# Kernel optimization log

Hardware: AMD Instinct MI355X
Metric: run time of the kernel (lower is better)

## Reference

```python
import jax, jax.numpy as jnp
import numpy as np

V_BOOK, V_AUTH, V_LANG, V_TAG = 10001, 5001, 28, 34253
D = 32  # EMBED_DIM
B, C, LH, LW = 4096, 100, 200, 50


def setup_inputs() -> dict:
    key = jax.random.key(0)
    ks = jax.random.split(key, 32)
    it = iter(ks)

    def emb(k, v):
        t = jax.random.normal(k, (v, D), jnp.float32) * 0.05
        return t.at[0].set(0.0)  # padding_idx=0

    def lin(k, i, o):
        k1, k2 = jax.random.split(k)
        lim = 1.0 / np.sqrt(i)
        return (jax.random.uniform(k1, (i, o), jnp.float32, -lim, lim),
                jax.random.uniform(k2, (o,), jnp.float32, -lim, lim))

    hist = jax.random.randint(next(it), (B, LH), 0, V_BOOK)
    wish = jax.random.randint(next(it), (B, LW), 0, V_BOOK)
    cand = jax.random.randint(next(it), (B, C), 0, V_BOOK)
    auth = jax.random.randint(next(it), (B, C), 0, V_AUTH)
    lang = jax.random.randint(next(it), (B, C), 0, V_LANG)
    tags = jax.random.randint(next(it), (B, C, 5), 0, V_TAG)
    dense = jax.random.normal(next(it), (B, C, 3), jnp.float32)

    E_hist = emb(next(it), V_BOOK)
    E_wish = emb(next(it), V_BOOK)
    E_cand = emb(next(it), V_BOOK)
    E_auth = emb(next(it), V_AUTH)
    E_lang = emb(next(it), V_LANG)
    E_tags = emb(next(it), V_TAG)

    Wb0, bb0 = lin(next(it), 3, 32)
    Wb1, bb1 = lin(next(it), 32, D)
    Wt0, bt0 = lin(next(it), 2 * D, 256)
    Wt1, bt1 = lin(next(it), 256, 128)
    Wt2, bt2 = lin(next(it), 128, 64)
    Wt3, bt3 = lin(next(it), 64, 1)

    return dict(hist=hist, wish=wish, cand=cand, auth=auth, lang=lang, tags=tags,
                dense=dense, E_hist=E_hist, E_wish=E_wish, E_cand=E_cand,
                E_auth=E_auth, E_lang=E_lang, E_tags=E_tags,
                Wb0=Wb0, bb0=bb0, Wb1=Wb1, bb1=bb1,
                Wt0=Wt0, bt0=bt0, Wt1=Wt1, bt1=bt1,
                Wt2=Wt2, bt2=bt2, Wt3=Wt3, bt3=bt3)


def reference(hist, wish, cand, auth, lang, tags, dense,
              E_hist, E_wish, E_cand, E_auth, E_lang, E_tags,
              Wb0, bb0, Wb1, bb1, Wt0, bt0, Wt1, bt1, Wt2, bt2, Wt3, bt3):
    # user side: mean-pooled history + wishlist embeddings  [B, D]
    u_vec = E_hist[hist].mean(axis=1) + E_wish[wish].mean(axis=1)
    # item side: candidate + author + language + mean of 5 tag embeddings  [B, C, D]
    e_t = E_tags[tags].sum(axis=2) / 5.0
    i_vec = E_cand[cand] + E_auth[auth] + E_lang[lang] + e_t
    # bottom MLP on dense features  [B, C, D]
    h = jax.nn.relu(jnp.einsum('bcf,fh->bch', dense, Wb0) + bb0)
    d_vec = jnp.einsum('bch,hd->bcd', h, Wb1) + bb1
    i_final = i_vec + d_vec
    # concat broadcast user vec with item vec  [B, C, 2D]
    u_exp = jnp.broadcast_to(u_vec[:, None, :], (u_vec.shape[0], i_final.shape[1], u_vec.shape[1]))
    x = jnp.concatenate([u_exp, i_final], axis=2)
    # top MLP -> scores [B, C]
    x = jax.nn.relu(x @ Wt0 + bt0)
    x = jax.nn.relu(x @ Wt1 + bt1)
    x = jax.nn.relu(x @ Wt2 + bt2)
    scores = (x @ Wt3 + bt3)[..., 0]
    return scores
```

## Files before the change

kernel.cpp:

```cpp
#include <hip/hip_runtime.h>
#include <hip/hip_bf16.h>
#include <stdint.h>

#define NB 4096
#define NC 100
#define NROWS (NB*NC)
#define NTILES (NROWS/64)
#define GRID_F 768
#define LH 200
#define LW 50

typedef short v8s __attribute__((ext_vector_type(8)));
typedef float v4f __attribute__((ext_vector_type(4)));
typedef float v2f __attribute__((ext_vector_type(2)));

__device__ __forceinline__ v4f mfma16(v8s a, v8s b, v4f c) {
  return __builtin_amdgcn_mfma_f32_16x16x32_bf16(a, b, c, 0, 0, 0);
}

__device__ __forceinline__ uint32_t pkbf(float lo, float hi) {
  uint32_t r;
  asm("v_cvt_pk_bf16_f32 %0, %1, %2" : "=v"(r) : "v"(lo), "v"(hi));
  return r;
}

__device__ __forceinline__ uint16_t bf16r(float f) {
  uint32_t u = __builtin_bit_cast(uint32_t, f);
  u = (u + 0x7fffu + ((u >> 16) & 1u)) >> 16;
  return (uint16_t)u;
}

__device__ __forceinline__ float bf2f(short s) {
  return __builtin_bit_cast(float, (uint32_t)((uint16_t)s) << 16);
}

__device__ __forceinline__ int ntli(const int* p) { return __builtin_nontemporal_load(p); }
__device__ __forceinline__ float ntlf(const float* p) { return __builtin_nontemporal_load(p); }

#define WS_FW 524288
#define FRAG_B1 0
#define FRAG_T0 2
#define FRAG_T1 34
#define FRAG_T2 98
#define NFRAGS 114

__global__ void k_prep(const float* __restrict__ Wb1, const float* __restrict__ Wt0,
                       const float* __restrict__ Wt1, const float* __restrict__ Wt2,
                       uint16_t* __restrict__ fb) {
  int f = blockIdx.x;
  int t = threadIdx.x;
  uint16_t res[2];
  #pragma unroll
  for (int e2 = 0; e2 < 2; ++e2) {
    int e = t * 2 + e2;
    int l = e >> 3, i = e & 7;
    int lr = l & 15, lg = l >> 4;
    float v;
    if (f < FRAG_T0) {
      v = Wb1[(lg * 8 + i) * 32 + 2 * lr + f];
    } else if (f < FRAG_T1) {
      int g = f - FRAG_T0;
      int wv = g >> 3, ch = (g >> 2) & 1, ks = (g >> 1) & 1, p = g & 1;
      int n = ch * 128 + wv * 32 + p * 16 + lr;
      int kl = ks * 32 + lg * 8 + i;
      v = Wt0[kl * 256 + n];
    } else if (f < FRAG_T2) {
      int g = f - FRAG_T1;
      int wv = g >> 4, ch = (g >> 3) & 1, ks = (g >> 1) & 3, p = g & 1;
      int n = wv * 32 + p * 16 + lr;
      int kl = ks * 32 + lg * 8 + i;
      int ok = ch * 128 + (kl & ~31) + ((kl & 31) >> 1) + ((kl & 1) << 4);
      v = Wt1[ok * 128 + n];
    } else {
      int g = f - FRAG_T2;
      int wv = g >> 2, ks = g & 3;
      int n = wv * 16 + lr;
      int kl = ks * 32 + lg * 8 + i;
      int ok = (kl & ~31) + ((kl & 31) >> 1) + ((kl & 1) << 4);
      v = Wt2[ok * 64 + n];
    }
    res[e2] = bf16r(v);
  }
  *(uint32_t*)(fb + (size_t)f * 512 + t * 2) = (uint32_t)res[0] | ((uint32_t)res[1] << 16);
}

__global__ void k_user(const int* __restrict__ hist, const int* __restrict__ wish,
                       const float* __restrict__ Eh, const float* __restrict__ Ew,
                       float* __restrict__ uv) {
  int t = threadIdx.x;
  int d = t & 31;
  int r = (blockIdx.x << 3) + (t >> 5);
  const int* hr = hist + r * LH;
  float s = 0.f;
  #pragma unroll 8
  for (int j = 0; j < LH; ++j) s += Eh[ntli(hr + j) * 32 + d];
  float su = s * (1.0f / LH);
  const int* wr = wish + r * LW;
  s = 0.f;
  #pragma unroll 5
  for (int j = 0; j < LW; ++j) s += Ew[ntli(wr + j) * 32 + d];
  uv[r * 32 + d] = su + s * (1.0f / LW);
}

#define SM_CONST 0
#define SM_X     2688
#define SM_ACT3  10880
#define SM_H     10880
#define SM_ACT   19072
#define SM_BYTES 35456

__global__ __launch_bounds__(256, 3)
void k_fused(const int* __restrict__ cand, const int* __restrict__ auth,
             const int* __restrict__ lang, const int* __restrict__ tags,
             const float* __restrict__ dense,
             const float* __restrict__ Ec, const float* __restrict__ Ea,
             const float* __restrict__ El, const float* __restrict__ Et,
             const float* __restrict__ Wb0, const float* __restrict__ bb0,
             const float* __restrict__ bb1, const float* __restrict__ bt0,
             const float* __restrict__ bt1, const float* __restrict__ bt2,
             const float* __restrict__ Wt3, const float* __restrict__ bt3,
             const float* __restrict__ uvec, const uint16_t* __restrict__ fw,
             float* __restrict__ out) {
  extern __shared__ char sm[];
  const char* fwp = (const char*)fw;
  float* cf = (float*)(sm + SM_CONST);
  const int t = threadIdx.x;
  const int l = t & 63, wv = t >> 6;
  const int lr = l & 15, lg = l >> 4;
  const int q = t & 3, rowl = t >> 2;

  cf[32 + t] = bt0[t];
  if (t < 128) cf[288 + t] = bt1[t];
  if (t < 64)  { cf[416 + t] = bt2[t]; cf[608 + t] = Wt3[t]; }
  if (t < 32)  { cf[t] = bb1[t]; cf[480 + t] = bb0[t]; }
  if (t < 96)  cf[512 + t] = Wb0[t];
  const float bt3v = bt3[0];

  for (int tile = blockIdx.x; tile < NTILES; tile += GRID_F) {
    const int r0 = tile << 6;
    __syncthreads();

    {
      int r = r0 + rowl;
      int b = r / 100;
      const float* up = uvec + b * 32 + q * 8;
      int xrb = SM_X + rowl * 128;
      int sw  = (rowl & 7) << 4;
      #pragma unroll
      for (int u2 = 0; u2 < 4; ++u2)
        *(uint32_t*)(sm + xrb + ((q * 16 + u2 * 4) ^ sw)) = pkbf(up[u2 * 2], up[u2 * 2 + 1]);
      float d0 = ntlf(dense + r * 3 + 0), d1 = ntlf(dense + r * 3 + 1), d2 = ntlf(dense + r * 3 + 2);
      const float* bb0l = cf + 480;
      const float* w0a = cf + 512, *w0b = cf + 544, *w0c = cf + 576;
      int hrb = SM_H + rowl * 64;
      int sw3 = (rowl & 3) << 4;
      #pragma unroll
      for (int u2 = 0; u2 < 4; ++u2) {
        int e0 = q * 8 + u2 * 2, e1 = e0 + 1;
        float h0 = fmaxf(bb0l[e0] + d0 * w0a[e0] + d1 * w0b[e0] + d2 * w0c[e0], 0.f);
        float h1 = fmaxf(bb0l[e1] + d0 * w0a[e1] + d1 * w0b[e1] + d2 * w0c[e1], 0.f);
        *(uint32_t*)(sm + hrb + ((q * 16 + u2 * 4) ^ sw3)) = pkbf(h0, h1);
      }
    }
    __syncthreads();

    {
      int hrow = 16 * wv + lr;
      v8s ah  = *(const v8s*)(sm + SM_H + hrow * 64 + ((lg * 16) ^ ((hrow & 3) << 4)));
      v8s wbl = *(const v8s*)(fwp + (size_t)(FRAG_B1 + 0) * 1024 + l * 16);
      v8s wbh = *(const v8s*)(fwp + (size_t)(FRAG_B1 + 1) * 1024 + l * 16);
      float b0v = cf[2 * lr], b1v = cf[2 * lr + 1];
      v4f dv0 = {b0v, b0v, b0v, b0v};
      v4f dv1 = {b1v, b1v, b1v, b1v};
      dv0 = mfma16(ah, wbl, dv0);
      dv1 = mfma16(ah, wbh, dv1);
      #pragma unroll
      for (int j = 0; j < 4; ++j) {
        int mrow = 16 * wv + lg * 4 + j;
        int rr = r0 + mrow;
        int ic = ntli(cand + rr), ia = ntli(auth + rr), il = ntli(lang + rr);
        const int* tp = tags + rr * 5;
        int t0i = ntli(tp), t1i = ntli(tp + 1), t2i = ntli(tp + 2), t3i = ntli(tp + 3), t4i = ntli(tp + 4);
        int co = 2 * lr;
        v2f ec = *(const v2f*)(Ec + ic * 32 + co);
        v2f ea = *(const v2f*)(Ea + ia * 32 + co);
        v2f el = *(const v2f*)(El + il * 32 + co);
        v2f e0 = *(const v2f*)(Et + t0i * 32 + co);
        v2f e1 = *(const v2f*)(Et + t1i * 32 + co);
        v2f e2 = *(const v2f*)(Et + t2i * 32 + co);
        v2f e3 = *(const v2f*)(Et + t3i * 32 + co);
        v2f e4 = *(const v2f*)(Et + t4i * 32 + co);
        float s0 = ec[0] + ea[0] + el[0] + (e0[0] + e1[0] + e2[0] + e3[0] + e4[0]) * 0.2f + dv0[j];
        float s1 = ec[1] + ea[1] + el[1] + (e0[1] + e1[1] + e2[1] + e3[1] + e4[1]) * 0.2f + dv1[j];
        *(uint32_t*)(sm + SM_X + mrow * 128 + ((64 + 4 * lr) ^ ((mrow & 7) << 4))) = pkbf(s0, s1);
      }
    }
    __syncthreads();

    v4f acc2[2][4];
    #pragma unroll
    for (int ch = 0; ch < 2; ++ch) {
      v4f a1[2][4];
      #pragma unroll
      for (int p = 0; p < 2; ++p) {
        float bv = cf[32 + ch * 128 + wv * 32 + p * 16 + lr];
        #pragma unroll
        for (int m = 0; m < 4; ++m) a1[p][m] = (v4f){bv, bv, bv, bv};
      }
      #pragma unroll
      for (int ks = 0; ks < 2; ++ks) {
        v8s xa[4];
        #pragma unroll
        for (int m = 0; m < 4; ++m)
          xa[m] = *(const v8s*)(sm + SM_X + (m * 16 + lr) * 128 + ((ks * 64 + lg * 16) ^ ((lr & 7) << 4)));
        #pragma unroll
        for (int p = 0; p < 2; ++p) {
          v8s wb = *(const v8s*)(fwp + (size_t)(FRAG_T0 + wv * 8 + ch * 4 + ks * 2 + p) * 1024 + l * 16);
          #pragma unroll
          for (int m = 0; m < 4; ++m) a1[p][m] = mfma16(xa[m], wb, a1[p][m]);
        }
      }
      #pragma unroll
      for (int m = 0; m < 4; ++m) {
        #pragma unroll
        for (int j = 0; j < 4; ++j) {
          int row = m * 16 + lg * 4 + j;
          *(uint32_t*)(sm + SM_ACT + row * 256 + ((wv * 64 + 4 * lr) ^ ((row & 7) << 4)))
            = pkbf(fmaxf(a1[0][m][j], 0.f), fmaxf(a1[1][m][j], 0.f));
        }
      }
      __syncthreads();
      if (ch == 0) {
        #pragma unroll
        for (int p = 0; p < 2; ++p) {
          float bv = cf[288 + wv * 32 + p * 16 + lr];
          #pragma unroll
          for (int m = 0; m < 4; ++m) acc2[p][m] = (v4f){bv, bv, bv, bv};
        }
      }
      #pragma unroll
      for (int ks = 0; ks < 4; ++ks) {
        v8s aa[4];
        #pragma unroll
        for (int m = 0; m < 4; ++m)
          aa[m] = *(const v8s*)(sm + SM_ACT + (m * 16 + lr) * 256 + ((ks * 64 + lg * 16) ^ ((lr & 7) << 4)));
        #pragma unroll
        for (int p = 0; p < 2; ++p) {
          v8s wb = *(const v8s*)(fwp + (size_t)(FRAG_T1 + wv * 16 + ch * 8 + ks * 2 + p) * 1024 + l * 16);
          #pragma unroll
          for (int m = 0; m < 4; ++m) acc2[p][m] = mfma16(aa[m], wb, acc2[p][m]);
        }
      }
      __syncthreads();
    }
    #pragma unroll
    for (int m = 0; m < 4; ++m) {
      #pragma unroll
      for (int j = 0; j < 4; ++j) {
        int row = m * 16 + lg * 4 + j;
        *(uint32_t*)(sm + SM_ACT + row * 256 + ((wv * 64 + 4 * lr) ^ ((row & 7) << 4)))
          = pkbf(fmaxf(acc2[0][m][j], 0.f), fmaxf(acc2[1][m][j], 0.f));
      }
    }
    __syncthreads();

    {
      int n2 = wv * 16 + lr;
      float bv = cf[416 + n2];
      v4f a3[4];
      #pragma unroll
      for (int m = 0; m < 4; ++m) a3[m] = (v4f){bv, bv, bv, bv};
      #pragma unroll
      for (int ks = 0; ks < 4; ++ks) {
        v8s wb = *(const v8s*)(fwp + (size_t)(FRAG_T2 + wv * 4 + ks) * 1024 + l * 16);
        #pragma unroll
        for (int m = 0; m < 4; ++m) {
          v8s aa = *(const v8s*)(sm + SM_ACT + (m * 16 + lr) * 256 + ((ks * 64 + lg * 16) ^ ((lr & 7) << 4)));
          a3[m] = mfma16(aa, wb, a3[m]);
        }
      }
      #pragma unroll
      for (int m = 0; m < 4; ++m) {
        #pragma unroll
        for (int j = 0; j < 4; ++j) {
          int row = m * 16 + lg * 4 + j;
          *(uint16_t*)(sm + SM_ACT3 + row * 128 + ((2 * n2) ^ ((row & 7) << 4))) = bf16r(fmaxf(a3[m][j], 0.f));
        }
      }
    }
    __syncthreads();

    {
      float acc = 0.f;
      int arb = SM_ACT3 + rowl * 128;
      int sw  = (rowl & 7) << 4;
      const float* wt3l = cf + 608;
      #pragma unroll
      for (int hf = 0; hf < 2; ++hf) {
        v8s av = *(const v8s*)(sm + arb + ((q * 32 + hf * 16) ^ sw));
        #pragma unroll
        for (int i = 0; i < 8; ++i) acc += bf2f(av[i]) * wt3l[q * 16 + hf * 8 + i];
      }
      acc += __shfl_xor(acc, 1);
      acc += __shfl_xor(acc, 2);
      if (q == 0) __builtin_nontemporal_store(acc + bt3v, out + r0 + rowl);
    }
  }
}

extern "C" void kernel_launch(void* const* d_in, const int* in_sizes, int n_in,
                              void* d_out, int out_size, void* d_ws, size_t ws_size,
                              hipStream_t stream) {
  const int*   hist  = (const int*)d_in[0];
  const int*   wish  = (const int*)d_in[1];
  const int*   cand  = (const int*)d_in[2];
  const int*   auth  = (const int*)d_in[3];
  const int*   lang  = (const int*)d_in[4];
  const int*   tags  = (const int*)d_in[5];
  const float* dense = (const float*)d_in[6];
  const float* Eh    = (const float*)d_in[7];
  const float* Ew    = (const float*)d_in[8];
  const float* Ec    = (const float*)d_in[9];
  const float* Ea    = (const float*)d_in[10];
  const float* El    = (const float*)d_in[11];
  const float* Et    = (const float*)d_in[12];
  const float* Wb0   = (const float*)d_in[13];
  const float* bb0   = (const float*)d_in[14];
  const float* Wb1   = (const float*)d_in[15];
  const float* bb1   = (const float*)d_in[16];
  const float* Wt0   = (const float*)d_in[17];
  const float* bt0   = (const float*)d_in[18];
  const float* Wt1   = (const float*)d_in[19];
  const float* bt1   = (const float*)d_in[20];
  const float* Wt2   = (const float*)d_in[21];
  const float* bt2   = (const float*)d_in[22];
  const float* Wt3   = (const float*)d_in[23];
  const float* bt3   = (const float*)d_in[24];
  char* wsb = (char*)d_ws;
  float* uv = (float*)wsb;
  uint16_t* fw = (uint16_t*)(wsb + WS_FW);
  float* out = (float*)d_out;

  (void)hipFuncSetAttribute((const void*)k_fused,
                            hipFuncAttributeMaxDynamicSharedMemorySize, SM_BYTES);

  k_prep<<<NFRAGS, 256, 0, stream>>>(Wb1, Wt0, Wt1, Wt2, fw);
  k_user<<<NB / 8, 256, 0, stream>>>(hist, wish, Eh, Ew, uv);
  k_fused<<<GRID_F, 256, SM_BYTES, stream>>>(cand, auth, lang, tags, dense,
      Ec, Ea, El, Et, Wb0, bb0, bb1, bt0, bt1, bt2, Wt3, bt3, uv, fw, out);
}
```

Before: 299.6 us.

## Gather item embeddings from bf16 tables and prefetch next-tile indices

```diff
diff --git a/kernel.cpp b/kernel.cpp
--- a/kernel.cpp
+++ b/kernel.cpp
@@ -6,7 +6,7 @@
 #define NC 100
 #define NROWS (NB*NC)
 #define NTILES (NROWS/64)
-#define GRID_F 768
+#define GRID_F 1024
 #define LH 200
 #define LW 50
 
@@ -33,16 +33,42 @@
 __device__ __forceinline__ float bf2f(short s) {
   return __builtin_bit_cast(float, (uint32_t)((uint16_t)s) << 16);
 }
+__device__ __forceinline__ float flo(uint32_t u) { return __builtin_bit_cast(float, u << 16); }
+__device__ __forceinline__ float fhi(uint32_t u) { return __builtin_bit_cast(float, u & 0xffff0000u); }
 
 __device__ __forceinline__ int ntli(const int* p) { return __builtin_nontemporal_load(p); }
 __device__ __forceinline__ float ntlf(const float* p) { return __builtin_nontemporal_load(p); }
 
-#define WS_FW 524288
+__device__ __forceinline__ void barx() {
+  asm volatile("s_waitcnt lgkmcnt(0)" ::: "memory");
+  __builtin_amdgcn_s_barrier();
+  asm volatile("" ::: "memory");
+}
+
+#define OFF_UV 0
+#define OFF_FW 524288
+#define OFF_TB 655360
+#define ET_BYTES (34253*64)
+#define EC_BYTES (10001*64)
+#define EA_BYTES (5001*64)
+#define EL_BYTES (28*64)
+
 #define FRAG_B1 0
 #define FRAG_T0 2
 #define FRAG_T1 34
 #define FRAG_T2 98
 #define NFRAGS 114
+
+__global__ void k_cvt1(const float* __restrict__ src, uint32_t* __restrict__ dst, int n8) {
+  int i = blockIdx.x * 256 + threadIdx.x;
+  if (i >= n8) return;
+  const float* p = src + (size_t)i * 8;
+  float4 a = *(const float4*)p;
+  float4 b = *(const float4*)(p + 4);
+  uint32_t* d = dst + (size_t)i * 4;
+  d[0] = pkbf(a.x, a.y); d[1] = pkbf(a.z, a.w);
+  d[2] = pkbf(b.x, b.y); d[3] = pkbf(b.z, b.w);
+}
 
 __global__ void k_prep(const float* __restrict__ Wb1, const float* __restrict__ Wt0,
                        const float* __restrict__ Wt1, const float* __restrict__ Wt2,
@@ -107,14 +133,17 @@
 #define SM_ACT3  10880
 #define SM_H     10880
 #define SM_ACT   19072
+#define SM_IDX   19072
 #define SM_BYTES 35456
 
-__global__ __launch_bounds__(256, 3)
+__global__ __launch_bounds__(256, 4)
 void k_fused(const int* __restrict__ cand, const int* __restrict__ auth,
              const int* __restrict__ lang, const int* __restrict__ tags,
              const float* __restrict__ dense,
              const float* __restrict__ Ec, const float* __restrict__ Ea,
              const float* __restrict__ El, const float* __restrict__ Et,
+             const uint16_t* __restrict__ EcB, const uint16_t* __restrict__ EaB,
+             const uint16_t* __restrict__ ElB, const uint16_t* __restrict__ EtB,
              const float* __restrict__ Wb0, const float* __restrict__ bb0,
              const float* __restrict__ bb1, const float* __restrict__ bt0,
              const float* __restrict__ bt1, const float* __restrict__ bt2,
@@ -136,20 +165,50 @@
   if (t < 96)  cf[512 + t] = Wb0[t];
   const float bt3v = bt3[0];
 
+  float4 uf0, uf1;
+  float d3x, d3y, d3z;
+  int i2a, i2b;
+
+  auto ld_tile = [&](int tl) {
+    int rr0 = (tl << 6) + rowl;
+    int b = rr0 / 100;
+    uf0 = *(const float4*)(uvec + b * 32 + q * 8);
+    uf1 = *(const float4*)(uvec + b * 32 + q * 8 + 4);
+    d3x = ntlf(dense + rr0 * 3 + 0);
+    d3y = ntlf(dense + rr0 * 3 + 1);
+    d3z = ntlf(dense + rr0 * 3 + 2);
+    int s0 = q * 2;
+    i2a = (s0 == 0) ? ntli(cand + rr0) : (s0 == 2) ? ntli(lang + rr0)
+        : (s0 == 4) ? ntli(tags + rr0 * 5 + 1) : ntli(tags + rr0 * 5 + 3);
+    i2b = (s0 == 0) ? ntli(auth + rr0) : (s0 == 2) ? ntli(tags + rr0 * 5 + 0)
+        : (s0 == 4) ? ntli(tags + rr0 * 5 + 2) : ntli(tags + rr0 * 5 + 4);
+  };
+
+  auto g2 = [&](const uint16_t* B, const float* F, int idx, float& a0, float& a1) {
+    if (B) {
+      uint32_t g = *(const uint32_t*)((const char*)B + ((size_t)idx << 6) + (lr << 2));
+      a0 = flo(g); a1 = fhi(g);
+    } else {
+      v2f e = *(const v2f*)(F + idx * 32 + 2 * lr);
+      a0 = e[0]; a1 = e[1];
+    }
+  };
+
+  ld_tile(blockIdx.x);
+
   for (int tile = blockIdx.x; tile < NTILES; tile += GRID_F) {
     const int r0 = tile << 6;
-    __syncthreads();
+    barx();
 
     {
-      int r = r0 + rowl;
-      int b = r / 100;
-      const float* up = uvec + b * 32 + q * 8;
       int xrb = SM_X + rowl * 128;
       int sw  = (rowl & 7) << 4;
-      #pragma unroll
-      for (int u2 = 0; u2 < 4; ++u2)
-        *(uint32_t*)(sm + xrb + ((q * 16 + u2 * 4) ^ sw)) = pkbf(up[u2 * 2], up[u2 * 2 + 1]);
-      float d0 = ntlf(dense + r * 3 + 0), d1 = ntlf(dense + r * 3 + 1), d2 = ntlf(dense + r * 3 + 2);
+      float uu[8] = {uf0.x, uf0.y, uf0.z, uf0.w, uf1.x, uf1.y, uf1.z, uf1.w};
+      #pragma unroll
+      for (int k2 = 0; k2 < 4; ++k2)
+        *(uint32_t*)(sm + xrb + ((q * 16 + k2 * 4) ^ sw)) = pkbf(uu[2*k2], uu[2*k2+1]);
+      *(int*)(sm + SM_IDX + rowl * 32 + q * 8)     = i2a;
+      *(int*)(sm + SM_IDX + rowl * 32 + q * 8 + 4) = i2b;
       const float* bb0l = cf + 480;
       const float* w0a = cf + 512, *w0b = cf + 544, *w0c = cf + 576;
       int hrb = SM_H + rowl * 64;
@@ -157,12 +216,14 @@
       #pragma unroll
       for (int u2 = 0; u2 < 4; ++u2) {
         int e0 = q * 8 + u2 * 2, e1 = e0 + 1;
-        float h0 = fmaxf(bb0l[e0] + d0 * w0a[e0] + d1 * w0b[e0] + d2 * w0c[e0], 0.f);
-        float h1 = fmaxf(bb0l[e1] + d0 * w0a[e1] + d1 * w0b[e1] + d2 * w0c[e1], 0.f);
+        float h0 = fmaxf(bb0l[e0] + d3x * w0a[e0] + d3y * w0b[e0] + d3z * w0c[e0], 0.f);
+        float h1 = fmaxf(bb0l[e1] + d3x * w0a[e1] + d3y * w0b[e1] + d3z * w0c[e1], 0.f);
         *(uint32_t*)(sm + hrb + ((q * 16 + u2 * 4) ^ sw3)) = pkbf(h0, h1);
       }
     }
-    __syncthreads();
+    barx();
+
+    if (tile + GRID_F < NTILES) ld_tile(tile + GRID_F);
 
     {
       int hrow = 16 * wv + lr;
@@ -177,25 +238,24 @@
       #pragma unroll
       for (int j = 0; j < 4; ++j) {
         int mrow = 16 * wv + lg * 4 + j;
-        int rr = r0 + mrow;
-        int ic = ntli(cand + rr), ia = ntli(auth + rr), il = ntli(lang + rr);
-        const int* tp = tags + rr * 5;
-        int t0i = ntli(tp), t1i = ntli(tp + 1), t2i = ntli(tp + 2), t3i = ntli(tp + 3), t4i = ntli(tp + 4);
-        int co = 2 * lr;
-        v2f ec = *(const v2f*)(Ec + ic * 32 + co);
-        v2f ea = *(const v2f*)(Ea + ia * 32 + co);
-        v2f el = *(const v2f*)(El + il * 32 + co);
-        v2f e0 = *(const v2f*)(Et + t0i * 32 + co);
-        v2f e1 = *(const v2f*)(Et + t1i * 32 + co);
-        v2f e2 = *(const v2f*)(Et + t2i * 32 + co);
-        v2f e3 = *(const v2f*)(Et + t3i * 32 + co);
-        v2f e4 = *(const v2f*)(Et + t4i * 32 + co);
-        float s0 = ec[0] + ea[0] + el[0] + (e0[0] + e1[0] + e2[0] + e3[0] + e4[0]) * 0.2f + dv0[j];
-        float s1 = ec[1] + ea[1] + el[1] + (e0[1] + e1[1] + e2[1] + e3[1] + e4[1]) * 0.2f + dv1[j];
+        const int* ip = (const int*)(sm + SM_IDX + mrow * 32);
+        int ic = ip[0], ia = ip[1], il = ip[2];
+        int t0i = ip[3], t1i = ip[4], t2i = ip[5], t3i = ip[6], t4i = ip[7];
+        float c0, c1, a0, a1, l0, l1, p0, p1, p2, p3, p4, p5, p6, p7, p8, p9;
+        g2(EcB, Ec, ic,  c0, c1);
+        g2(EaB, Ea, ia,  a0, a1);
+        g2(ElB, El, il,  l0, l1);
+        g2(EtB, Et, t0i, p0, p1);
+        g2(EtB, Et, t1i, p2, p3);
+        g2(EtB, Et, t2i, p4, p5);
+        g2(EtB, Et, t3i, p6, p7);
+        g2(EtB, Et, t4i, p8, p9);
+        float s0 = c0 + a0 + l0 + (p0 + p2 + p4 + p6 + p8) * 0.2f + dv0[j];
+        float s1 = c1 + a1 + l1 + (p1 + p3 + p5 + p7 + p9) * 0.2f + dv1[j];
         *(uint32_t*)(sm + SM_X + mrow * 128 + ((64 + 4 * lr) ^ ((mrow & 7) << 4))) = pkbf(s0, s1);
       }
     }
-    __syncthreads();
+    barx();
 
     v4f acc2[2][4];
     #pragma unroll
@@ -229,7 +289,7 @@
             = pkbf(fmaxf(a1[0][m][j], 0.f), fmaxf(a1[1][m][j], 0.f));
         }
       }
-      __syncthreads();
+      barx();
       if (ch == 0) {
         #pragma unroll
         for (int p = 0; p < 2; ++p) {
@@ -251,7 +311,7 @@
           for (int m = 0; m < 4; ++m) acc2[p][m] = mfma16(aa[m], wb, acc2[p][m]);
         }
       }
-      __syncthreads();
+      barx();
     }
     #pragma unroll
     for (int m = 0; m < 4; ++m) {
@@ -262,7 +322,7 @@
           = pkbf(fmaxf(acc2[0][m][j], 0.f), fmaxf(acc2[1][m][j], 0.f));
       }
     }
-    __syncthreads();
+    barx();
 
     {
       int n2 = wv * 16 + lr;
@@ -288,7 +348,7 @@
         }
       }
     }
-    __syncthreads();
+    barx();
 
     {
       float acc = 0.f;
@@ -303,7 +363,8 @@
       }
       acc += __shfl_xor(acc, 1);
       acc += __shfl_xor(acc, 2);
-      if (q == 0) __builtin_nontemporal_store(acc + bt3v, out + r0 + rowl);
+      float sc = __shfl(acc + bt3v, (l & 15) * 4);
+      if (l < 16) out[r0 + wv * 16 + l] = sc;
     }
   }
 }
@@ -337,15 +398,28 @@
   const float* Wt3   = (const float*)d_in[23];
   const float* bt3   = (const float*)d_in[24];
   char* wsb = (char*)d_ws;
-  float* uv = (float*)wsb;
-  uint16_t* fw = (uint16_t*)(wsb + WS_FW);
   float* out = (float*)d_out;
+
+  float*    uv = (float*)(wsb + OFF_UV);
+  uint16_t* fw = (uint16_t*)(wsb + OFF_FW);
+
+  size_t off = OFF_TB;
+  uint16_t *EtB = nullptr, *EcB = nullptr, *EaB = nullptr, *ElB = nullptr;
+  if (off + ET_BYTES <= ws_size) { EtB = (uint16_t*)(wsb + off); off += ET_BYTES; }
+  if (off + EC_BYTES <= ws_size) { EcB = (uint16_t*)(wsb + off); off += EC_BYTES; }
+  if (off + EA_BYTES <= ws_size) { EaB = (uint16_t*)(wsb + off); off += EA_BYTES; }
+  if (off + EL_BYTES <= ws_size) { ElB = (uint16_t*)(wsb + off); off += EL_BYTES; }
 
   (void)hipFuncSetAttribute((const void*)k_fused,
                             hipFuncAttributeMaxDynamicSharedMemorySize, SM_BYTES);
 
+  if (EtB) k_cvt1<<<(34253*4 + 255)/256, 256, 0, stream>>>(Et, (uint32_t*)EtB, 34253*4);
+  if (EcB) k_cvt1<<<(10001*4 + 255)/256, 256, 0, stream>>>(Ec, (uint32_t*)EcB, 10001*4);
+  if (EaB) k_cvt1<<<(5001*4 + 255)/256, 256, 0, stream>>>(Ea, (uint32_t*)EaB, 5001*4);
+  if (ElB) k_cvt1<<<1, 256, 0, stream>>>(El, (uint32_t*)ElB, 28*4);
   k_prep<<<NFRAGS, 256, 0, stream>>>(Wb1, Wt0, Wt1, Wt2, fw);
   k_user<<<NB / 8, 256, 0, stream>>>(hist, wish, Eh, Ew, uv);
   k_fused<<<GRID_F, 256, SM_BYTES, stream>>>(cand, auth, lang, tags, dense,
-      Ec, Ea, El, Et, Wb0, bb0, bb1, bt0, bt1, bt2, Wt3, bt3, uv, fw, out);
-}
+      Ec, Ea, El, Et, EcB, EaB, ElB, EtB, Wb0, bb0, bb1, bt0, bt1, bt2, Wt3, bt3,
+      uv, fw, out);
+}
```

Result: slower. 385.8 us (+28.8%).
